# Kernel optimization log

Hardware: AMD Instinct MI355X
Metric: run time of the kernel (lower is better)

Reference implementation:

```python
import jax, jax.numpy as jnp
import numpy as np

ENT_SIZE = 100000; REL_SIZE = 500; ENT_DIM = 256; REL_DIM = 256; H = 256
E = 2048; S = 32; N = 1024; THRESHOLD = 1.0; EPS = 1e-5


def _xav(k, shape):
    fan_in = shape[-1]
    fan_out = shape[-2] if len(shape) > 1 else shape[-1]
    std = (2.0 / (fan_in + fan_out)) ** 0.5
    return jax.random.normal(k, shape, jnp.float32) * std


def setup_inputs() -> dict:
    key = jax.random.key(0)
    ks = jax.random.split(key, 16)
    inp = {}
    inp["neighbors"] = jax.random.randint(ks[0], (E, S), 0, ENT_SIZE)
    inp["pos_h"] = jax.random.randint(ks[1], (N,), 0, E)
    inp["pos_t"] = jax.random.randint(ks[2], (N,), 0, E)
    inp["pos_r"] = jax.random.randint(ks[3], (N,), 0, REL_SIZE)
    inp["neg_h"] = jax.random.randint(ks[4], (N,), 0, E)
    inp["neg_t"] = jax.random.randint(ks[5], (N,), 0, E)
    inp["neg_r"] = jax.random.randint(ks[6], (N,), 0, REL_SIZE)
    inp["ent_embed"] = _xav(ks[7], (ENT_SIZE + 1, ENT_DIM))
    inp["rel_embed"] = _xav(ks[8], (REL_SIZE, REL_DIM))
    inp["trans"] = _xav(ks[9], (2 * REL_SIZE, REL_DIM, ENT_DIM))
    inp["W_ih_f"] = _xav(ks[10], (4 * H, ENT_DIM)); inp["W_hh_f"] = _xav(ks[11], (4 * H, H))
    inp["W_ih_b"] = _xav(ks[12], (4 * H, ENT_DIM)); inp["W_hh_b"] = _xav(ks[13], (4 * H, H))
    inp["b_f"] = jnp.zeros((4 * H,), jnp.float32)
    inp["b_b"] = jnp.zeros((4 * H,), jnp.float32)
    inp["W_lin"] = _xav(ks[14], (ENT_DIM, 2 * H)); inp["b_lin"] = jnp.zeros((ENT_DIM,), jnp.float32)
    inp["gamma"] = jnp.ones((ENT_DIM,), jnp.float32); inp["beta"] = jnp.zeros((ENT_DIM,), jnp.float32)
    return inp


def _lstm_final(x, W_ih, W_hh, b):
    # x: [E,S,D] -> final hidden state [E,H] (PyTorch LSTM gate order i,f,g,o; b = b_ih+b_hh)
    h0 = jnp.zeros((x.shape[0], H), x.dtype)
    def step(carry, xt):
        h, c = carry
        g = xt @ W_ih.T + h @ W_hh.T + b  # [E,4H]
        i, f, gg, o = jnp.split(g, 4, axis=-1)
        c = jax.nn.sigmoid(f) * c + jax.nn.sigmoid(i) * jnp.tanh(gg)
        h = jax.nn.sigmoid(o) * jnp.tanh(c)
        return (h, c), None
    (h, _), _ = jax.lax.scan(step, (h0, h0), jnp.swapaxes(x, 0, 1))
    return h


def _context(ent_embed, neighbors, W_ih_f, W_hh_f, b_f, W_ih_b, W_hh_b, b_b, W_lin, b_lin, gamma, beta):
    x_seq = ent_embed[neighbors]  # [E,S,D]
    h_f = _lstm_final(x_seq, W_ih_f, W_hh_f, b_f)
    h_b = _lstm_final(x_seq[:, ::-1], W_ih_b, W_hh_b, b_b)
    lin = jnp.concatenate([h_f, h_b], -1) @ W_lin.T + b_lin  # [E,ENT_DIM]
    # BatchNorm1d in training mode: batch stats (biased variance)
    mu = lin.mean(0)
    var = lin.var(0)
    return jnp.tanh(gamma * (lin - mu) * jax.lax.rsqrt(var + EPS) + beta)


def _score(trans, rel_embed, ctx, h_idx, r_idx, t_idx):
    Wh = trans[r_idx]             # [N,REL_DIM,ENT_DIM] (grouped expert GEMV, batched)
    Wt = trans[r_idx + REL_SIZE]
    d = jnp.einsum('nre,ne->nr', Wh, ctx[h_idx]) - jnp.einsum('nre,ne->nr', Wt, ctx[t_idx])
    return jnp.linalg.norm(d + rel_embed[r_idx], axis=1)


def reference(neighbors, pos_h, pos_t, pos_r, neg_h, neg_t, neg_r,
              ent_embed, rel_embed, trans, W_ih_f, W_hh_f, W_ih_b, W_hh_b,
              b_f, b_b, W_lin, b_lin, gamma, beta):
    ctx = _context(ent_embed, neighbors, W_ih_f, W_hh_f, b_f, W_ih_b, W_hh_b, b_b,
                   W_lin, b_lin, gamma, beta)
    pos_n = _score(trans, rel_embed, ctx, pos_h, pos_r, pos_t)
    neg_n = _score(trans, rel_embed, ctx, neg_h, neg_r, neg_t)
    return jnp.sum(pos_n + jax.nn.relu(THRESHOLD - neg_n))
```

## Files before the change

kernel.cpp:

```cpp
#include <hip/hip_runtime.h>

constexpr int kE   = 2048;
constexpr int kS   = 32;
constexpr int kD   = 256;
constexpr int kK   = 512;
constexpr int kREL = 500;
constexpr int kN   = 1024;

typedef unsigned short u16;
typedef __attribute__((ext_vector_type(8))) _Float16 f16x8;
typedef __attribute__((ext_vector_type(4))) float    f32x4;
typedef __attribute__((ext_vector_type(4))) unsigned short us4;

static __device__ __forceinline__ u16 f2h(float f) {
  _Float16 h = (_Float16)f;
  return __builtin_bit_cast(u16, h);
}
static __device__ __forceinline__ float h2f(u16 v) {
  _Float16 h = __builtin_bit_cast(_Float16, v);
  return (float)h;
}
static __device__ __forceinline__ float sigf(float x) { return 1.f / (1.f + __expf(-x)); }
static __device__ __forceinline__ float tanhfast(float x) {
  float e = __expf(2.f * x);
  return 1.f - 2.f / (e + 1.f);
}
static __device__ __forceinline__ void gl_lds16(const void* g, void* l) {
  __builtin_amdgcn_global_load_lds((const __attribute__((address_space(1))) unsigned int*)g,
                                   (__attribute__((address_space(3))) unsigned int*)l, 16, 0, 0);
}

__global__ void prep_gather(const float* __restrict__ Wih_f, const float* __restrict__ Whh_f,
                            const float* __restrict__ Wih_b, const float* __restrict__ Whh_b,
                            const float* __restrict__ Wlin_in,
                            const int* __restrict__ neighbors, const float* __restrict__ ent,
                            u16* __restrict__ Wv3, u16* __restrict__ Whhr,
                            u16* __restrict__ Wlin, u16* __restrict__ ximg) {
  if (blockIdx.x < 576) {
    int idx = blockIdx.x * 256 + threadIdx.x;
    if (idx < 65536) {
      int q  = idx & 2047;
      int ch = (idx >> 11) & 3;
      int y  = (idx >> 13) & 3;
      int d  = idx >> 15;
      int j  = q >> 3;
      int k8 = (q & 7) ^ (j & 7);
      int jg = y * 256 + j;
      int g = (jg >> 4) & 3, u = (jg >> 6) * 16 + (jg & 15);
      int R = g * 256 + u;
      int k = ch * 64 + k8 * 8;
      const float* src = (d ? Wih_b : Wih_f) + R * 256 + k;
      ushort oa[8];
#pragma unroll
      for (int i = 0; i < 8; i++) oa[i] = f2h(src[i]);
      *(uint4*)((char*)Wv3 + (size_t)idx * 16) = *(uint4*)oa;
    } else if (idx < 131072) {
      int i2 = idx - 65536;
      int d = i2 >> 15;
      int j = (i2 & 32767) >> 5;
      int k = (i2 & 31) * 8;
      int g = (j >> 4) & 3, u = (j >> 6) * 16 + (j & 15);
      int R = g * 256 + u;
      const float* src = (d ? Whh_b : Whh_f) + R * 256 + k;
      ushort oa[8];
#pragma unroll
      for (int i = 0; i < 8; i++) oa[i] = f2h(src[i]);
      *(uint4*)((char*)Whhr + (size_t)i2 * 16) = *(uint4*)oa;
    } else if (idx < 131072 + 16384) {
      int q = (idx - 131072) * 8;
#pragma unroll
      for (int i = 0; i < 8; i++) Wlin[q + i] = f2h(Wlin_in[q + i]);
    }
  } else {
    int idx = (blockIdx.x - 576) * 256 + threadIdx.x;
    int q    = idx & 511;
    int ch   = (idx >> 9) & 3;
    int tile = (idx >> 11) & 31;
    int s    = idx >> 16;
    int row = q >> 3;
    int c8 = (q & 7) ^ (row & 7);
    int e = tile * 64 + row;
    int k = ch * 64 + c8 * 8;
    int nb = neighbors[e * 32 + s];
    const float* src = ent + (size_t)nb * 256 + k;
    float4 v0 = *(const float4*)src;
    float4 v1 = *(const float4*)(src + 4);
    ushort oa[8];
    oa[0] = f2h(v0.x); oa[1] = f2h(v0.y); oa[2] = f2h(v0.z); oa[3] = f2h(v0.w);
    oa[4] = f2h(v1.x); oa[5] = f2h(v1.y); oa[6] = f2h(v1.z); oa[7] = f2h(v1.w);
    *(uint4*)((char*)ximg + (size_t)idx * 16) = *(uint4*)oa;
  }
}

__global__ __launch_bounds__(256) void xgemm(
    const u16* __restrict__ ximg, const u16* __restrict__ Wv3,
    const float* __restrict__ b_f, const float* __restrict__ b_b,
    u16* __restrict__ gx) {
  __shared__ __align__(16) char As[8192];
  __shared__ __align__(16) char Bs[32768];
  const int tid = threadIdx.x, lane = tid & 63, w = tid >> 6;
  const int l15 = lane & 15, lq = lane >> 4;
  const int ts = blockIdx.x >> 5;
  const int etile = blockIdx.x & 31;
  const int y = blockIdx.y, dir = blockIdx.z;
  const int e0 = etile * 64;
  const int s = dir ? (31 - ts) : ts;
  const char* imgA = (const char*)ximg + (size_t)(s * 32 + etile) * 32768;
  const char* imgB = (const char*)Wv3 + (size_t)(dir * 4 + y) * 131072;
  const float* bd = dir ? b_b : b_f;
  const int u = (y * 4 + w) * 16 + l15;

  f32x4 acc[4][4];
#pragma unroll
  for (int n = 0; n < 4; n++) {
    float bv = bd[n * 256 + u];
#pragma unroll
    for (int m = 0; m < 4; m++) acc[m][n] = (f32x4){bv, bv, bv, bv};
  }

  for (int ch = 0; ch < 4; ++ch) {
#pragma unroll
    for (int i = 0; i < 2; i++)
      gl_lds16(imgA + ch * 8192 + i * 4096 + w * 1024 + lane * 16,
               As + i * 4096 + w * 1024);
#pragma unroll
    for (int i = 0; i < 8; i++)
      gl_lds16(imgB + (size_t)ch * 32768 + i * 4096 + w * 1024 + lane * 16,
               Bs + i * 4096 + w * 1024);
    __syncthreads();
#pragma unroll
    for (int ks = 0; ks < 2; ++ks) {
      const int kb = ks * 64 + lq * 16;
      f16x8 a[4], b[4];
#pragma unroll
      for (int m = 0; m < 4; m++) {
        int row = m * 16 + l15;
        a[m] = *(const f16x8*)(As + row * 128 + (kb ^ ((row & 7) << 4)));
      }
#pragma unroll
      for (int n = 0; n < 4; n++) {
        int row = w * 64 + n * 16 + l15;
        b[n] = *(const f16x8*)(Bs + row * 128 + (kb ^ ((row & 7) << 4)));
      }
#pragma unroll
      for (int m = 0; m < 4; m++)
#pragma unroll
        for (int n = 0; n < 4; n++)
          acc[m][n] = __builtin_amdgcn_mfma_f32_16x16x32_f16(a[m], b[n], acc[m][n], 0, 0, 0);
    }
    __syncthreads();
  }

  u16* out = gx + ((size_t)(dir * kS + ts) * kE) * 1024;
#pragma unroll
  for (int m = 0; m < 4; m++)
#pragma unroll
    for (int r = 0; r < 4; r++) {
      int e = e0 + m * 16 + lq * 4 + r;
      us4 o;
      o[0] = f2h(acc[m][0][r]); o[1] = f2h(acc[m][1][r]);
      o[2] = f2h(acc[m][2][r]); o[3] = f2h(acc[m][3][r]);
      __builtin_nontemporal_store(o, (us4*)(out + ((size_t)e * 256 + u) * 4));
    }
}

__global__ __launch_bounds__(256) void lstm_step(
    const u16* __restrict__ gx, const u16* __restrict__ Whhr,
    const u16* __restrict__ hprev, u16* __restrict__ hnext,
    float* __restrict__ cbuf, int t) {
  const int tid = threadIdx.x, lane = tid & 63, w = tid >> 6;
  const int l15 = lane & 15, lq = lane >> 4;
  const int bid = blockIdx.x;
  const int dir = bid >> 8;
  const int rem = bid & 255;
  const int jg = rem >> 6;
  const int et = rem & 63;
  const int e0 = et * 32;
  const int c0 = jg * 256 + w * 64;
  const int unit = (c0 >> 6) * 16 + l15;

  const u16* Wd  = Whhr + ((size_t)dir * 1024 + c0) * kD;
  const u16* hpd = hprev + (size_t)dir * kE * kD;
  u16* hnd = hnext + (size_t)dir * kE * kD;
  float* cd = cbuf + (size_t)dir * kE * kD;
  const u16* gp = gx + ((size_t)(dir * kS + t) * kE) * 1024;

  f32x4 acc[2][4];
#pragma unroll
  for (int m = 0; m < 2; m++)
#pragma unroll
    for (int r = 0; r < 4; r++) {
      us4 g = __builtin_nontemporal_load(
          (const us4*)(gp + (size_t)(e0 + m * 16 + lq * 4 + r) * 1024 + unit * 4));
#pragma unroll
      for (int n = 0; n < 4; n++) acc[m][n][r] = h2f(g[n]);
    }

  const int klane = lq * 8;
#pragma unroll
  for (int ks = 0; ks < 8; ks++) {
    const int ka = ks * 32 + klane;
    f16x8 a[2], b[4];
#pragma unroll
    for (int m = 0; m < 2; m++)
      a[m] = *(const f16x8*)(hpd + (size_t)(e0 + m * 16 + l15) * kD + ka);
#pragma unroll
    for (int n = 0; n < 4; n++)
      b[n] = *(const f16x8*)(Wd + (size_t)(n * 16 + l15) * kD + ka);
#pragma unroll
    for (int m = 0; m < 2; m++)
#pragma unroll
      for (int n = 0; n < 4; n++)
        acc[m][n] = __builtin_amdgcn_mfma_f32_16x16x32_f16(a[m], b[n], acc[m][n], 0, 0, 0);
  }

#pragma unroll
  for (int m = 0; m < 2; m++)
#pragma unroll
    for (int r = 0; r < 4; r++) {
      int row = e0 + m * 16 + lq * 4 + r;
      size_t off = (size_t)row * kD + unit;
      float gi = acc[m][0][r];
      float gf = acc[m][1][r];
      float gg = acc[m][2][r];
      float go = acc[m][3][r];
      float c_old = cd[off];
      float cn = sigf(gf) * c_old + sigf(gi) * tanhfast(gg);
      cd[off] = cn;
      hnd[off] = f2h(sigf(go) * tanhfast(cn));
    }
}

static __device__ __forceinline__ void gemm_tile(
    const u16* __restrict__ Alo, const u16* __restrict__ Ahi,
    const u16* __restrict__ W, int e0,
    u16* As, u16* Bs, f32x4 (&acc)[4][4]) {
  const int tid = threadIdx.x;
  const int lane = tid & 63;
  const int w = tid >> 6;
#pragma unroll
  for (int m = 0; m < 4; m++)
#pragma unroll
    for (int n = 0; n < 4; n++) acc[m][n] = (f32x4){0.f, 0.f, 0.f, 0.f};

  for (int ch = 0; ch < 8; ++ch) {
    const int k0 = ch * 64;
    __syncthreads();
    const u16* Asrc = (k0 < 256) ? Alo : Ahi;
    const int kbase = (k0 < 256) ? k0 : (k0 - 256);
#pragma unroll
    for (int i = 0; i < 2; i++) {
      int idx = tid + i * 256;
      int row = idx >> 3, c8 = idx & 7;
      uint4 v = *(const uint4*)(Asrc + (size_t)(e0 + row) * 256 + kbase + c8 * 8);
      *(uint4*)((char*)As + row * 128 + ((c8 * 16) ^ ((row & 7) << 4))) = v;
    }
#pragma unroll
    for (int i = 0; i < 8; i++) {
      int idx = tid + i * 256;
      int j = idx >> 3, c8 = idx & 7;
      uint4 v = *(const uint4*)(W + (size_t)j * kK + k0 + c8 * 8);
      *(uint4*)((char*)Bs + j * 128 + ((c8 * 16) ^ ((j & 7) << 4))) = v;
    }
    __syncthreads();
#pragma unroll
    for (int ks = 0; ks < 2; ++ks) {
      const int kb = ks * 64 + (lane >> 4) * 16;
      f16x8 a[4], b[4];
#pragma unroll
      for (int m = 0; m < 4; m++) {
        int row = m * 16 + (lane & 15);
        a[m] = *(const f16x8*)((const char*)As + row * 128 + (kb ^ ((row & 7) << 4)));
      }
#pragma unroll
      for (int n = 0; n < 4; n++) {
        int row = w * 64 + n * 16 + (lane & 15);
        b[n] = *(const f16x8*)((const char*)Bs + row * 128 + (kb ^ ((row & 7) << 4)));
      }
#pragma unroll
      for (int m = 0; m < 4; m++)
#pragma unroll
        for (int n = 0; n < 4; n++)
          acc[m][n] = __builtin_amdgcn_mfma_f32_16x16x32_f16(a[m], b[n], acc[m][n], 0, 0, 0);
    }
  }
}

__global__ __launch_bounds__(256) void lin_kernel(
    const u16* __restrict__ hf, const u16* __restrict__ hb,
    const u16* __restrict__ Wl, const float* __restrict__ b_lin,
    float* __restrict__ lin, float* __restrict__ part) {
  __shared__ __align__(16) char smem[40960];
  u16* As = (u16*)smem;
  u16* Bs = (u16*)(smem + 8192);
  const int tid = threadIdx.x, lane = tid & 63, w = tid >> 6;
  const int l15 = lane & 15, lq = lane >> 4;
  const int e0 = blockIdx.x * 64;
  f32x4 acc[4][4];
  gemm_tile(hf, hb, Wl, e0, As, Bs, acc);
#pragma unroll
  for (int n = 0; n < 4; n++) {
    int col = w * 64 + n * 16 + l15;
    float bl = b_lin[col];
    float s1 = 0.f, s2 = 0.f;
#pragma unroll
    for (int m = 0; m < 4; m++)
#pragma unroll
      for (int r = 0; r < 4; r++) {
        int e = e0 + m * 16 + lq * 4 + r;
        float v = acc[m][n][r] + bl;
        lin[(size_t)e * 256 + col] = v;
        s1 += v; s2 += v * v;
      }
    s1 += __shfl_down(s1, 16); s2 += __shfl_down(s2, 16);
    s1 += __shfl_down(s1, 32); s2 += __shfl_down(s2, 32);
    if (lq == 0) {
      part[blockIdx.x * 256 + col] = s1;
      part[8192 + blockIdx.x * 256 + col] = s2;
    }
  }
}

__global__ void bn_apply(const float* __restrict__ lin, const float* __restrict__ part,
                         const float* __restrict__ gamma, const float* __restrict__ beta,
                         float* __restrict__ ctx) {
  int c = threadIdx.x;
  float s = 0.f, s2 = 0.f;
  for (int b = 0; b < 32; b++) { s += part[b * 256 + c]; s2 += part[8192 + b * 256 + c]; }
  float mu = s * (1.f / 2048.f);
  float rsig = rsqrtf(s2 * (1.f / 2048.f) - mu * mu + 1e-5f);
  float ga = gamma[c], be = beta[c];
  int e0 = blockIdx.x * 8;
  for (int e = e0; e < e0 + 8; ++e) {
    float x = lin[(size_t)e * 256 + c];
    ctx[(size_t)e * 256 + c] = tanhf(ga * (x - mu) * rsig + be);
  }
}

__global__ void group_rel(const int* __restrict__ pr, const int* __restrict__ nr,
                          int* __restrict__ offs, int* __restrict__ list) {
  __shared__ int cnt[512], sc[512], cur[512];
  int tid = threadIdx.x;
  cnt[tid] = 0;
  __syncthreads();
  for (int i = tid; i < 2 * kN; i += 512) {
    int r = (i < kN) ? pr[i] : nr[i - kN];
    atomicAdd(&cnt[r], 1);
  }
  __syncthreads();
  sc[tid] = cnt[tid];
  __syncthreads();
  for (int d = 1; d < 512; d <<= 1) {
    int v = (tid >= d) ? sc[tid - d] : 0;
    __syncthreads();
    sc[tid] += v;
    __syncthreads();
  }
  int excl = (tid == 0) ? 0 : sc[tid - 1];
  cur[tid] = excl;
  if (tid <= kREL) offs[tid] = excl;
  __syncthreads();
  for (int i = tid; i < 2 * kN; i += 512) {
    int r = (i < kN) ? pr[i] : nr[i - kN];
    int p = atomicAdd(&cur[r], 1);
    list[p] = i;
  }
}

template <int NJ>
static __device__ __forceinline__ void score_body(
    const float* __restrict__ ctx, const float* __restrict__ trans,
    const float* __restrict__ rel_embed,
    const int* __restrict__ ph, const int* __restrict__ pt,
    const int* __restrict__ nh, const int* __restrict__ nt,
    const int* __restrict__ list, float* __restrict__ sqacc,
    int r, int half, int start, int G,
    float* csh, float* cst, float (*red)[4], int* tidx) {
  const int tid = threadIdx.x;
#pragma unroll
  for (int j = 0; j < NJ; j++) {
    float vh = 0.f, vt = 0.f;
    if (j < G) {
      int i = list[start + j];
      int hh = (i < kN) ? ph[i] : nh[i - kN];
      int tt = (i < kN) ? pt[i] : nt[i - kN];
      vh = ctx[(size_t)hh * 256 + tid];
      vt = ctx[(size_t)tt * 256 + tid];
      if (tid == 0) tidx[j] = i;
    }
    csh[j * 256 + tid] = vh;
    cst[j * 256 + tid] = vt;
  }
  __syncthreads();

  const int row = half * 128 + (tid >> 1);
  const int q4b = (tid & 1) * 32;
  const float4* whp = (const float4*)(trans + (size_t)r * 65536 + (size_t)row * 256) + q4b;
  const float4* wtp = (const float4*)(trans + ((size_t)r + kREL) * 65536 + (size_t)row * 256) + q4b;
  const float4* ch4 = (const float4*)csh;
  const float4* ct4 = (const float4*)cst;

  float acc[NJ];
#pragma unroll
  for (int j = 0; j < NJ; j++) acc[j] = 0.f;

  for (int line = 0; line < 4; line++) {
    float4 wh[8], wt[8];
#pragma unroll
    for (int i = 0; i < 8; i++) { wh[i] = whp[line * 8 + i]; wt[i] = wtp[line * 8 + i]; }
#pragma unroll
    for (int q4 = 0; q4 < 8; q4++) {
      const int qa = q4b + line * 8 + q4;
#pragma unroll
      for (int j = 0; j < NJ; j++) {
        float4 xh = ch4[j * 64 + qa];
        float4 xt = ct4[j * 64 + qa];
        acc[j] += wh[q4].x * xh.x + wh[q4].y * xh.y + wh[q4].z * xh.z + wh[q4].w * xh.w
                - (wt[q4].x * xt.x + wt[q4].y * xt.y + wt[q4].z * xt.z + wt[q4].w * xt.w);
      }
    }
  }

  const float rv = rel_embed[r * 256 + row];
#pragma unroll
  for (int j = 0; j < NJ; j++) {
    float d = acc[j] + __shfl_xor(acc[j], 1) + rv;
    float v = d * d;
    v += __shfl_down(v, 32); v += __shfl_down(v, 16);
    v += __shfl_down(v, 8);  v += __shfl_down(v, 4);
    v += __shfl_down(v, 2);  v += __shfl_down(v, 1);
    if ((tid & 63) == 0) red[j][tid >> 6] = v;
  }
  __syncthreads();
  if (tid < G) {
    float s = (red[tid][0] + red[tid][1] + red[tid][2] + red[tid][3]) * 0.5f;
    atomicAdd(&sqacc[tidx[tid]], s);
  }
  __syncthreads();
}

__global__ __launch_bounds__(256) void score_grouped(
    const float* __restrict__ ctx, const float* __restrict__ trans,
    const float* __restrict__ rel_embed,
    const int* __restrict__ ph, const int* __restrict__ pt,
    const int* __restrict__ nh, const int* __restrict__ nt,
    const int* __restrict__ offs, const int* __restrict__ list,
    float* __restrict__ sqacc) {
  const int r = blockIdx.x >> 1, half = blockIdx.x & 1;
  int start = offs[r], end = offs[r + 1];
  if (start >= end) return;
  __shared__ float csh[16 * 256];
  __shared__ float cst[16 * 256];
  __shared__ float red[16][4];
  __shared__ int tidx[16];
  for (int c = start; c < end; c += 16) {
    int G = min(16, end - c);
    if (G <= 4)
      score_body<4>(ctx, trans, rel_embed, ph, pt, nh, nt, list, sqacc, r, half, c, G,
                    csh, cst, red, tidx);
    else if (G <= 8)
      score_body<8>(ctx, trans, rel_embed, ph, pt, nh, nt, list, sqacc, r, half, c, G,
                    csh, cst, red, tidx);
    else
      score_body<16>(ctx, trans, rel_embed, ph, pt, nh, nt, list, sqacc, r, half, c, G,
                     csh, cst, red, tidx);
  }
}

__global__ void final_reduce(const float* __restrict__ sqacc, float* __restrict__ out) {
  int tid = threadIdx.x;
  float a = 0.f;
  for (int i = tid; i < 2 * kN; i += 256) {
    float s = sqrtf(sqacc[i]);
    a += (i < kN) ? s : fmaxf(0.f, 1.f - s);
  }
  for (int off = 32; off; off >>= 1) a += __shfl_down(a, off);
  __shared__ float w4[4];
  if ((tid & 63) == 0) w4[tid >> 6] = a;
  __syncthreads();
  if (tid == 0) out[0] = w4[0] + w4[1] + w4[2] + w4[3];
}

extern "C" void kernel_launch(void* const* d_in, const int* in_sizes, int n_in,
                              void* d_out, int out_size, void* d_ws, size_t ws_size,
                              hipStream_t stream) {
  const int*   neighbors = (const int*)d_in[0];
  const int*   pos_h = (const int*)d_in[1];
  const int*   pos_t = (const int*)d_in[2];
  const int*   pos_r = (const int*)d_in[3];
  const int*   neg_h = (const int*)d_in[4];
  const int*   neg_t = (const int*)d_in[5];
  const int*   neg_r = (const int*)d_in[6];
  const float* ent_embed = (const float*)d_in[7];
  const float* rel_embed = (const float*)d_in[8];
  const float* trans = (const float*)d_in[9];
  const float* W_ih_f = (const float*)d_in[10];
  const float* W_hh_f = (const float*)d_in[11];
  const float* W_ih_b = (const float*)d_in[12];
  const float* W_hh_b = (const float*)d_in[13];
  const float* b_f = (const float*)d_in[14];
  const float* b_b = (const float*)d_in[15];
  const float* W_lin = (const float*)d_in[16];
  const float* b_lin = (const float*)d_in[17];
  const float* gamma = (const float*)d_in[18];
  const float* beta = (const float*)d_in[19];

  char* ws = (char*)d_ws;
  size_t off = 0;
  auto alloc = [&](size_t bytes) {
    void* p = ws + off;
    off = (off + bytes + 255) & ~(size_t)255;
    return p;
  };
  u16* Wv3    = (u16*)alloc((size_t)65536 * 16);
  u16* Whhr   = (u16*)alloc((size_t)2 * 1024 * kD * 2);
  u16* Wlin   = (u16*)alloc((size_t)256 * kK * 2);
  u16* ximg   = (u16*)alloc((size_t)2097152 * 16);
  u16* h0     = (u16*)alloc((size_t)2 * kE * kD * 2);
  u16* h1     = (u16*)alloc((size_t)2 * kE * kD * 2);
  float* cbuf = (float*)alloc((size_t)2 * kE * kD * 4);
  u16* gx     = (u16*)alloc((size_t)2 * kS * kE * 1024 * 2);
  float* lin  = (float*)alloc((size_t)kE * 256 * 4);
  float* part = (float*)alloc((size_t)2 * 32 * 256 * 4);
  float* ctx  = (float*)alloc((size_t)kE * 256 * 4);
  float* sqacc = (float*)alloc((size_t)2 * kN * 4);
  int* offsb  = (int*)alloc((size_t)512 * 4);
  int* list   = (int*)alloc((size_t)2 * kN * 4);
  (void)in_sizes; (void)n_in; (void)out_size; (void)ws_size;

  hipMemsetAsync(h0, 0, (size_t)2 * kE * kD * 2, stream);
  hipMemsetAsync(cbuf, 0, (size_t)2 * kE * kD * 4, stream);
  hipMemsetAsync(sqacc, 0, (size_t)2 * kN * 4, stream);

  prep_gather<<<576 + 8192, 256, 0, stream>>>(W_ih_f, W_hh_f, W_ih_b, W_hh_b, W_lin,
                                              neighbors, ent_embed,
                                              Wv3, Whhr, Wlin, ximg);
  group_rel<<<1, 512, 0, stream>>>(pos_r, neg_r, offsb, list);

  xgemm<<<dim3(1024, 4, 2), 256, 0, stream>>>(ximg, Wv3, b_f, b_b, gx);

  for (int t = 0; t < kS; t++) {
    const u16* hp = (t & 1) ? h1 : h0;
    u16* hn = (t & 1) ? h0 : h1;
    lstm_step<<<512, 256, 0, stream>>>(gx, Whhr, hp, hn, cbuf, t);
  }

  lin_kernel<<<32, 256, 0, stream>>>(h0, h0 + (size_t)kE * kD, Wlin, b_lin, lin, part);
  bn_apply<<<256, 256, 0, stream>>>(lin, part, gamma, beta, ctx);
  score_grouped<<<2 * kREL, 256, 0, stream>>>(ctx, trans, rel_embed,
                                              pos_h, pos_t, neg_h, neg_t, offsb, list, sqacc);
  final_reduce<<<1, 256, 0, stream>>>(sqacc, (float*)d_out);
}
```

Before: 804.9 us.

## Enlarge LSTM step tiles to 2x2 warp grid and fuse final reduce into scoring

After: 788.2 us. 2.1% less time.

```diff
diff --git a/kernel.cpp b/kernel.cpp
--- a/kernel.cpp
+++ b/kernel.cpp
@@ -171,23 +171,23 @@
   const int tid = threadIdx.x, lane = tid & 63, w = tid >> 6;
   const int l15 = lane & 15, lq = lane >> 4;
   const int bid = blockIdx.x;
-  const int dir = bid >> 8;
-  const int rem = bid & 255;
-  const int jg = rem >> 6;
-  const int et = rem & 63;
-  const int e0 = et * 32;
-  const int c0 = jg * 256 + w * 64;
+  const int dir = bid >> 7;
+  const int ut  = (bid >> 4) & 7;
+  const int et  = bid & 15;
+  const int wr = w >> 1, wc = w & 1;
+  const int e0 = et * 128 + wr * 64;
+  const int c0 = ut * 128 + wc * 64;
   const int unit = (c0 >> 6) * 16 + l15;
 
-  const u16* Wd  = Whhr + ((size_t)dir * 1024 + c0) * kD;
+  const u16* Wd  = Whhr + (size_t)dir * 1024 * kD;
   const u16* hpd = hprev + (size_t)dir * kE * kD;
   u16* hnd = hnext + (size_t)dir * kE * kD;
   float* cd = cbuf + (size_t)dir * kE * kD;
   const u16* gp = gx + ((size_t)(dir * kS + t) * kE) * 1024;
 
-  f32x4 acc[2][4];
-#pragma unroll
-  for (int m = 0; m < 2; m++)
+  f32x4 acc[4][4];
+#pragma unroll
+  for (int m = 0; m < 4; m++)
 #pragma unroll
     for (int r = 0; r < 4; r++) {
       us4 g = __builtin_nontemporal_load(
@@ -200,22 +200,22 @@
 #pragma unroll
   for (int ks = 0; ks < 8; ks++) {
     const int ka = ks * 32 + klane;
-    f16x8 a[2], b[4];
-#pragma unroll
-    for (int m = 0; m < 2; m++)
+    f16x8 a[4], b[4];
+#pragma unroll
+    for (int m = 0; m < 4; m++)
       a[m] = *(const f16x8*)(hpd + (size_t)(e0 + m * 16 + l15) * kD + ka);
 #pragma unroll
     for (int n = 0; n < 4; n++)
-      b[n] = *(const f16x8*)(Wd + (size_t)(n * 16 + l15) * kD + ka);
-#pragma unroll
-    for (int m = 0; m < 2; m++)
+      b[n] = *(const f16x8*)(Wd + (size_t)(c0 + n * 16 + l15) * kD + ka);
+#pragma unroll
+    for (int m = 0; m < 4; m++)
 #pragma unroll
       for (int n = 0; n < 4; n++)
         acc[m][n] = __builtin_amdgcn_mfma_f32_16x16x32_f16(a[m], b[n], acc[m][n], 0, 0, 0);
   }
 
 #pragma unroll
-  for (int m = 0; m < 2; m++)
+  for (int m = 0; m < 4; m++)
 #pragma unroll
     for (int r = 0; r < 4; r++) {
       int row = e0 + m * 16 + lq * 4 + r;
@@ -445,40 +445,51 @@
     const int* __restrict__ ph, const int* __restrict__ pt,
     const int* __restrict__ nh, const int* __restrict__ nt,
     const int* __restrict__ offs, const int* __restrict__ list,
-    float* __restrict__ sqacc) {
+    float* __restrict__ sqacc, int* __restrict__ done,
+    float* __restrict__ out) {
   const int r = blockIdx.x >> 1, half = blockIdx.x & 1;
   int start = offs[r], end = offs[r + 1];
-  if (start >= end) return;
   __shared__ float csh[16 * 256];
   __shared__ float cst[16 * 256];
   __shared__ float red[16][4];
   __shared__ int tidx[16];
-  for (int c = start; c < end; c += 16) {
-    int G = min(16, end - c);
-    if (G <= 4)
-      score_body<4>(ctx, trans, rel_embed, ph, pt, nh, nt, list, sqacc, r, half, c, G,
-                    csh, cst, red, tidx);
-    else if (G <= 8)
-      score_body<8>(ctx, trans, rel_embed, ph, pt, nh, nt, list, sqacc, r, half, c, G,
-                    csh, cst, red, tidx);
-    else
-      score_body<16>(ctx, trans, rel_embed, ph, pt, nh, nt, list, sqacc, r, half, c, G,
-                     csh, cst, red, tidx);
-  }
-}
-
-__global__ void final_reduce(const float* __restrict__ sqacc, float* __restrict__ out) {
-  int tid = threadIdx.x;
-  float a = 0.f;
-  for (int i = tid; i < 2 * kN; i += 256) {
-    float s = sqrtf(sqacc[i]);
-    a += (i < kN) ? s : fmaxf(0.f, 1.f - s);
-  }
-  for (int off = 32; off; off >>= 1) a += __shfl_down(a, off);
+  __shared__ int lastBlock;
   __shared__ float w4[4];
-  if ((tid & 63) == 0) w4[tid >> 6] = a;
-  __syncthreads();
-  if (tid == 0) out[0] = w4[0] + w4[1] + w4[2] + w4[3];
+
+  if (start < end) {
+    for (int c = start; c < end; c += 16) {
+      int G = min(16, end - c);
+      if (G <= 4)
+        score_body<4>(ctx, trans, rel_embed, ph, pt, nh, nt, list, sqacc, r, half, c, G,
+                      csh, cst, red, tidx);
+      else if (G <= 8)
+        score_body<8>(ctx, trans, rel_embed, ph, pt, nh, nt, list, sqacc, r, half, c, G,
+                      csh, cst, red, tidx);
+      else
+        score_body<16>(ctx, trans, rel_embed, ph, pt, nh, nt, list, sqacc, r, half, c, G,
+                       csh, cst, red, tidx);
+    }
+  }
+
+  if (threadIdx.x == 0) {
+    __threadfence();
+    int old = atomicAdd(done, 1);
+    lastBlock = (old == 2 * kREL - 1) ? 1 : 0;
+  }
+  __syncthreads();
+  if (lastBlock) {
+    __threadfence();
+    int tid = threadIdx.x;
+    float a = 0.f;
+    for (int i = tid; i < 2 * kN; i += 256) {
+      float s = sqrtf(sqacc[i]);
+      a += (i < kN) ? s : fmaxf(0.f, 1.f - s);
+    }
+    for (int o = 32; o; o >>= 1) a += __shfl_down(a, o);
+    if ((tid & 63) == 0) w4[tid >> 6] = a;
+    __syncthreads();
+    if (tid == 0) out[0] = w4[0] + w4[1] + w4[2] + w4[3];
+  }
 }
 
 extern "C" void kernel_launch(void* const* d_in, const int* in_sizes, int n_in,
@@ -526,11 +537,13 @@
   float* sqacc = (float*)alloc((size_t)2 * kN * 4);
   int* offsb  = (int*)alloc((size_t)512 * 4);
   int* list   = (int*)alloc((size_t)2 * kN * 4);
+  int* done   = (int*)alloc((size_t)256);
   (void)in_sizes; (void)n_in; (void)out_size; (void)ws_size;
 
   hipMemsetAsync(h0, 0, (size_t)2 * kE * kD * 2, stream);
   hipMemsetAsync(cbuf, 0, (size_t)2 * kE * kD * 4, stream);
   hipMemsetAsync(sqacc, 0, (size_t)2 * kN * 4, stream);
+  hipMemsetAsync(done, 0, (size_t)256, stream);
 
   prep_gather<<<576 + 8192, 256, 0, stream>>>(W_ih_f, W_hh_f, W_ih_b, W_hh_b, W_lin,
                                               neighbors, ent_embed,
@@ -542,12 +555,12 @@
   for (int t = 0; t < kS; t++) {
     const u16* hp = (t & 1) ? h1 : h0;
     u16* hn = (t & 1) ? h0 : h1;
-    lstm_step<<<512, 256, 0, stream>>>(gx, Whhr, hp, hn, cbuf, t);
+    lstm_step<<<256, 256, 0, stream>>>(gx, Whhr, hp, hn, cbuf, t);
   }
 
   lin_kernel<<<32, 256, 0, stream>>>(h0, h0 + (size_t)kE * kD, Wlin, b_lin, lin, part);
   bn_apply<<<256, 256, 0, stream>>>(lin, part, gamma, beta, ctx);
   score_grouped<<<2 * kREL, 256, 0, stream>>>(ctx, trans, rel_embed,
-                                              pos_h, pos_t, neg_h, neg_t, offsb, list, sqacc);
-  final_reduce<<<1, 256, 0, stream>>>(sqacc, (float*)d_out);
-}
+                                              pos_h, pos_t, neg_h, neg_t, offsb, list,
+                                              sqacc, done, (float*)d_out);
+}
```
